# Performance work log

Hardware: AMD Instinct MI355X
Metric: run time of the kernel (lower is better)

The kernel has to match this reference:

```python
import jax, jax.numpy as jnp
import numpy as np

N_NODES = 50000
N_EDGES = 800000
NFEAT = 128
NHID = 128
BN_EPS = 1e-5


def setup_inputs() -> dict:
    key = jax.random.key(0)
    ks = jax.random.split(key, 8)
    x = jax.random.normal(ks[0], (N_NODES, NFEAT), dtype=jnp.float32)
    edge_index = jax.random.randint(ks[1], (2, N_EDGES), 0, N_NODES, dtype=jnp.int64)
    # Linear weights in torch layout [out, in]; scaled like kaiming-ish init.
    W1 = jax.random.normal(ks[2], (NHID, NFEAT), dtype=jnp.float32) / np.sqrt(NFEAT)
    b1 = jax.random.normal(ks[3], (NHID,), dtype=jnp.float32) * 0.01
    gamma = jnp.ones((NHID,), dtype=jnp.float32)
    beta = jnp.zeros((NHID,), dtype=jnp.float32)
    W2 = jax.random.normal(ks[4], (NHID, NHID), dtype=jnp.float32) / np.sqrt(NHID)
    b2 = jax.random.normal(ks[5], (NHID,), dtype=jnp.float32) * 0.01
    return {"x": x, "edge_index": edge_index, "W1": W1, "b1": b1,
            "gamma": gamma, "beta": beta, "W2": W2, "b2": b2}


def reference(x, edge_index, W1, b1, gamma, beta, W2, b2):
    # GINConv, eps = 0: h = (1 + eps) * x + sum_{j in N(i)} x_j
    src, dst = edge_index[0], edge_index[1]
    agg = x + jax.ops.segment_sum(x[src], dst, num_segments=N_NODES)  # [N, nfeat]
    # MLP: Linear -> ReLU -> BatchNorm1d (training stats) -> Linear
    h = jnp.maximum(agg @ W1.T + b1, 0.0)                             # [N, nhid]
    mean = jnp.mean(h, axis=0)
    var = jnp.var(h, axis=0)  # biased variance, as torch BN uses for normalization
    h = (h - mean) * jax.lax.rsqrt(var + BN_EPS) * gamma + beta
    return h @ W2.T + b2
```

## Files before the change

### kernel.cpp

```cpp
#include <hip/hip_runtime.h>

#define N_NODES 50000
#define N_EDGES 800000
#define NF 128
#define BN_EPS 1e-5f
#define G_ROWS 32
#define GBLOCKS ((N_NODES + G_ROWS - 1) / G_ROWS)
#define NB 1568
#define SCAN_BLOCKS ((N_NODES + 255) / 256)
#define AP 136
#define HP 132

typedef __attribute__((ext_vector_type(8))) short short8;
typedef __attribute__((ext_vector_type(4))) float f32x4;

__device__ __forceinline__ unsigned short f2bf(float f) {
    union { float f; unsigned int i; } v; v.f = f;
    unsigned int r = (v.i + 0x7fffu + ((v.i >> 16) & 1u)) >> 16;
    return (unsigned short)r;
}
__device__ __forceinline__ float bf2f(unsigned short u) {
    union { unsigned int i; float f; } v; v.i = ((unsigned int)u) << 16; return v.f;
}

#define SETUP_C (N_NODES * NF / 4)
#define SETUP_P (128 * 128)
#define SETUP_Z N_NODES
#define SETUP_S 256
__global__ void setup_kernel(const float* __restrict__ x, unsigned short* __restrict__ xb,
                             const float* __restrict__ W1, const float* __restrict__ W2,
                             unsigned short* __restrict__ Wb1, unsigned short* __restrict__ Wb2,
                             int* __restrict__ counts, float* __restrict__ stats,
                             int do_convert) {
    int i = blockIdx.x * blockDim.x + threadIdx.x;
    int off = do_convert ? 0 : SETUP_C;
    i += off;
    if (i < SETUP_C) {
        float4 v = ((const float4*)x)[i];
        ushort4 u;
        u.x = f2bf(v.x); u.y = f2bf(v.y); u.z = f2bf(v.z); u.w = f2bf(v.w);
        ((ushort4*)xb)[i] = u;
    } else if (i < SETUP_C + SETUP_P) {
        int j = i - SETUP_C;
        Wb1[j] = f2bf(W1[j]);
        Wb2[j] = f2bf(W2[j]);
    } else if (i < SETUP_C + SETUP_P + SETUP_Z) {
        counts[i - SETUP_C - SETUP_P] = 0;
    } else if (i < SETUP_C + SETUP_P + SETUP_Z + SETUP_S) {
        stats[i - SETUP_C - SETUP_P - SETUP_Z] = 0.0f;
    }
}

__global__ void hist_kernel(const int* __restrict__ ei, int* __restrict__ counts,
                            int* __restrict__ rank) {
    int t = blockIdx.x * blockDim.x + threadIdx.x;
    if (t < N_EDGES) rank[t] = atomicAdd(&counts[ei[N_EDGES + t]], 1);
}

__global__ __launch_bounds__(256) void scan_reduce(const int* __restrict__ counts,
                                                   int* __restrict__ partials) {
    __shared__ int red[256];
    int t = threadIdx.x;
    int i = blockIdx.x * 256 + t;
    red[t] = (i < N_NODES) ? counts[i] : 0;
    __syncthreads();
    for (int off = 128; off > 0; off >>= 1) {
        if (t < off) red[t] += red[t + off];
        __syncthreads();
    }
    if (t == 0) partials[blockIdx.x] = red[0];
}

__global__ __launch_bounds__(256) void scan_partials2(int* __restrict__ partials) {
    __shared__ int s[256];
    int t = threadIdx.x;
    int v = (t < SCAN_BLOCKS) ? partials[t] : 0;
    s[t] = v;
    __syncthreads();
    for (int off = 1; off < 256; off <<= 1) {
        int u = (t >= off) ? s[t - off] : 0;
        __syncthreads();
        s[t] += u;
        __syncthreads();
    }
    if (t < SCAN_BLOCKS) partials[t] = s[t] - v;
}

__global__ __launch_bounds__(256) void scan_apply(const int* __restrict__ counts,
                                                  const int* __restrict__ partials,
                                                  int* __restrict__ rowptr) {
    __shared__ int s[256];
    int t = threadIdx.x;
    int i = blockIdx.x * 256 + t;
    int v = (i < N_NODES) ? counts[i] : 0;
    s[t] = v;
    __syncthreads();
    for (int off = 1; off < 256; off <<= 1) {
        int u = (t >= off) ? s[t - off] : 0;
        __syncthreads();
        s[t] += u;
        __syncthreads();
    }
    int excl = partials[blockIdx.x] + s[t] - v;
    if (i < N_NODES) rowptr[i] = excl;
    if (i == 0) rowptr[N_NODES] = N_EDGES;
}

__global__ void fill_kernel(const int* __restrict__ ei,
                            const int* __restrict__ rowptr,
                            const int* __restrict__ rank,
                            int* __restrict__ ssrc) {
    int t = blockIdx.x * blockDim.x + threadIdx.x;
    if (t < N_EDGES) {
        int dst = ei[N_EDGES + t];
        ssrc[rowptr[dst] + rank[t]] = ei[t];
    }
}

__global__ __launch_bounds__(256) void gather_bf16(const unsigned short* __restrict__ xb,
                                                   const int* __restrict__ rowptr,
                                                   const int* __restrict__ ssrc,
                                                   unsigned short* __restrict__ buf) {
    int node = (blockIdx.x * blockDim.x + threadIdx.x) >> 6;
    int lane = threadIdx.x & 63;
    if (node >= N_NODES) return;
    const unsigned int* x2 = (const unsigned int*)xb;
    unsigned int u = x2[(size_t)node * 64 + lane];
    float ax = bf2f((unsigned short)(u & 0xffffu));
    float ay = bf2f((unsigned short)(u >> 16));
    int beg = rowptr[node], end = rowptr[node + 1];
    int e = beg;
    for (; e + 3 < end; e += 4) {
        int s0 = ssrc[e], s1 = ssrc[e + 1], s2 = ssrc[e + 2], s3 = ssrc[e + 3];
        unsigned int u0 = x2[(size_t)s0 * 64 + lane];
        unsigned int u1 = x2[(size_t)s1 * 64 + lane];
        unsigned int u2 = x2[(size_t)s2 * 64 + lane];
        unsigned int u3 = x2[(size_t)s3 * 64 + lane];
        ax += bf2f((unsigned short)(u0 & 0xffffu)) + bf2f((unsigned short)(u1 & 0xffffu))
            + bf2f((unsigned short)(u2 & 0xffffu)) + bf2f((unsigned short)(u3 & 0xffffu));
        ay += bf2f((unsigned short)(u0 >> 16)) + bf2f((unsigned short)(u1 >> 16))
            + bf2f((unsigned short)(u2 >> 16)) + bf2f((unsigned short)(u3 >> 16));
    }
    for (; e < end; e++) {
        unsigned int u0 = x2[(size_t)ssrc[e] * 64 + lane];
        ax += bf2f((unsigned short)(u0 & 0xffffu));
        ay += bf2f((unsigned short)(u0 >> 16));
    }
    unsigned int packed = ((unsigned int)f2bf(ay) << 16) | (unsigned int)f2bf(ax);
    ((unsigned int*)buf)[(size_t)node * 64 + lane] = packed;
}

__global__ __launch_bounds__(256) void gemm1_bf16(
    unsigned short* __restrict__ buf,
    const unsigned short* __restrict__ Wb,
    const float* __restrict__ b1,
    float* __restrict__ P) {
    __shared__ unsigned short At[G_ROWS][AP];
    __shared__ float Ht[G_ROWS][HP];

    int t = threadIdx.x;
    int base = blockIdx.x * G_ROWS;
    int nrows = N_NODES - base; if (nrows > G_ROWS) nrows = G_ROWS;

    for (int i = t; i < G_ROWS * 16; i += 256) {
        int r = i >> 4, c8 = i & 15;
        uint4 v = make_uint4(0u, 0u, 0u, 0u);
        if (r < nrows) v = ((const uint4*)(buf + (size_t)(base + r) * NF))[c8];
        *((uint4*)&At[r][c8 * 8]) = v;
    }
    __syncthreads();

    int wave = t >> 6, lane = t & 63;
    int m0 = (wave & 1) * 16;
    int n0 = (wave >> 1) * 64;
    int l15 = lane & 15, q = lane >> 4;

    f32x4 acc[4];
#pragma unroll
    for (int i = 0; i < 4; i++) acc[i] = (f32x4){0.f, 0.f, 0.f, 0.f};

#pragma unroll
    for (int kc = 0; kc < 4; kc++) {
        short8 a = *((const short8*)&At[m0 + l15][kc * 32 + q * 8]);
#pragma unroll
        for (int tile = 0; tile < 4; tile++) {
            short8 b = *((const short8*)(Wb + (size_t)(n0 + 16 * tile + l15) * 128 + kc * 32 + q * 8));
            acc[tile] = __builtin_amdgcn_mfma_f32_16x16x32_bf16(a, b, acc[tile], 0, 0, 0);
        }
    }

#pragma unroll
    for (int tile = 0; tile < 4; tile++) {
        int col = n0 + 16 * tile + l15;
        float bias = b1[col];
#pragma unroll
        for (int reg = 0; reg < 4; reg++) {
            int row = q * 4 + reg;
            Ht[m0 + row][col] = fmaxf(acc[tile][reg] + bias, 0.f);
        }
    }
    __syncthreads();

    for (int i = t; i < G_ROWS * 32; i += 256) {
        int r = i >> 5, c4 = i & 31;
        int row = base + r;
        if (row < N_NODES) {
            float4 v = *((const float4*)&Ht[r][c4 * 4]);
            ushort4 u;
            u.x = f2bf(v.x); u.y = f2bf(v.y); u.z = f2bf(v.z); u.w = f2bf(v.w);
            *((ushort4*)(buf + (size_t)row * NF + c4 * 4)) = u;
        }
    }

    {
        int f = t & 127;
        bool issq = (t >= 128);
        float s = 0.f;
        for (int r = 0; r < nrows; r++) {
            float v = Ht[r][f];
            s += issq ? v * v : v;
        }
        P[(size_t)t * NB + blockIdx.x] = s;
    }
}

__global__ __launch_bounds__(256) void bn_reduce(const float* __restrict__ P,
                                                 const float* __restrict__ gamma,
                                                 const float* __restrict__ beta,
                                                 float* __restrict__ ab) {
    __shared__ float s1[256], s2[256];
    int f = blockIdx.x;
    int j = threadIdx.x;
    float a = 0.f, b = 0.f;
    for (int k = j; k < GBLOCKS; k += 256) {
        a += P[(size_t)f * NB + k];
        b += P[(size_t)(128 + f) * NB + k];
    }
    s1[j] = a; s2[j] = b;
    __syncthreads();
    for (int off = 128; off > 0; off >>= 1) {
        if (j < off) { s1[j] += s1[j + off]; s2[j] += s2[j + off]; }
        __syncthreads();
    }
    if (j == 0) {
        float mean = s1[0] * (1.0f / N_NODES);
        float var = s2[0] * (1.0f / N_NODES) - mean * mean;
        float rstd = rsqrtf(var + BN_EPS);
        float aa = gamma[f] * rstd;
        float cc = beta[f] - mean * aa;
        ab[f] = aa;
        ab[128 + f] = cc;
    }
}

__global__ __launch_bounds__(256) void gemm2_bf16(
    const unsigned short* __restrict__ buf,
    const unsigned short* __restrict__ Wb,
    const float* __restrict__ b2,
    const float* __restrict__ ab,
    float* __restrict__ out) {
    __shared__ unsigned short At[G_ROWS][AP];
    __shared__ float Ht[G_ROWS][HP];

    int t = threadIdx.x;
    int base = blockIdx.x * G_ROWS;
    int nrows = N_NODES - base; if (nrows > G_ROWS) nrows = G_ROWS;

    for (int i = t; i < G_ROWS * 32; i += 256) {
        int r = i >> 5, c4 = i & 31;
        ushort4 u = make_ushort4(0, 0, 0, 0);
        if (r < nrows) {
            ushort4 hv = *((const ushort4*)(buf + (size_t)(base + r) * NF + c4 * 4));
            float4 av = ((const float4*)ab)[c4];
            float4 cv = ((const float4*)(ab + 128))[c4];
            u.x = f2bf(bf2f(hv.x) * av.x + cv.x);
            u.y = f2bf(bf2f(hv.y) * av.y + cv.y);
            u.z = f2bf(bf2f(hv.z) * av.z + cv.z);
            u.w = f2bf(bf2f(hv.w) * av.w + cv.w);
        }
        *((ushort4*)&At[r][c4 * 4]) = u;
    }
    __syncthreads();

    int wave = t >> 6, lane = t & 63;
    int m0 = (wave & 1) * 16;
    int n0 = (wave >> 1) * 64;
    int l15 = lane & 15, q = lane >> 4;

    f32x4 acc[4];
#pragma unroll
    for (int i = 0; i < 4; i++) acc[i] = (f32x4){0.f, 0.f, 0.f, 0.f};

#pragma unroll
    for (int kc = 0; kc < 4; kc++) {
        short8 a = *((const short8*)&At[m0 + l15][kc * 32 + q * 8]);
#pragma unroll
        for (int tile = 0; tile < 4; tile++) {
            short8 b = *((const short8*)(Wb + (size_t)(n0 + 16 * tile + l15) * 128 + kc * 32 + q * 8));
            acc[tile] = __builtin_amdgcn_mfma_f32_16x16x32_bf16(a, b, acc[tile], 0, 0, 0);
        }
    }

#pragma unroll
    for (int tile = 0; tile < 4; tile++) {
        int col = n0 + 16 * tile + l15;
        float bias = b2[col];
#pragma unroll
        for (int reg = 0; reg < 4; reg++) {
            int row = q * 4 + reg;
            Ht[m0 + row][col] = acc[tile][reg] + bias;
        }
    }
    __syncthreads();

    for (int i = t; i < G_ROWS * 32; i += 256) {
        int r = i >> 5, c4 = i & 31;
        int row = base + r;
        if (row < N_NODES)
            *((float4*)(out + (size_t)row * NF + c4 * 4)) = *((const float4*)&Ht[r][c4 * 4]);
    }
}

__global__ void finalize_bn(const float* __restrict__ stats,
                            const float* __restrict__ gamma,
                            const float* __restrict__ beta,
                            float* __restrict__ ab) {
    int f = threadIdx.x;
    if (f < 128) {
        float mean = stats[f] * (1.0f / N_NODES);
        float var = stats[128 + f] * (1.0f / N_NODES) - mean * mean;
        float rstd = rsqrtf(var + BN_EPS);
        float a = gamma[f] * rstd;
        float c = beta[f] - mean * a;
        ab[f] = a;
        ab[128 + f] = c;
    }
}

__global__ __launch_bounds__(256) void fused_gather_gemm1_f32(
    const float* __restrict__ xv,
    const int* __restrict__ rowptr,
    const int* __restrict__ ssrc,
    const unsigned short* __restrict__ Wb,
    const float* __restrict__ b1,
    float* __restrict__ hout,
    float* __restrict__ stats) {
    __shared__ unsigned short At[G_ROWS][AP];
    __shared__ float Ht[G_ROWS][HP];

    int t = threadIdx.x;
    int wave = t >> 6, lane = t & 63;
    int base = blockIdx.x * G_ROWS;
    int nrows = N_NODES - base; if (nrows > G_ROWS) nrows = G_ROWS;

    const float2* xf2 = (const float2*)xv;

    for (int nn = 0; nn < 8; nn++) {
        int r = wave * 8 + nn;
        int node = base + r;
        float2 acc = make_float2(0.f, 0.f);
        if (node < N_NODES) {
            acc = xf2[(size_t)node * 64 + lane];
            int beg = rowptr[node], end = rowptr[node + 1];
            for (int e = beg; e < end; e++) {
                float2 v0 = xf2[(size_t)ssrc[e] * 64 + lane];
                acc.x += v0.x;
                acc.y += v0.y;
            }
        }
        unsigned int packed = ((unsigned int)f2bf(acc.y) << 16) | (unsigned int)f2bf(acc.x);
        *((unsigned int*)&At[r][lane * 2]) = packed;
    }
    __syncthreads();

    int m0 = (wave & 1) * 16;
    int n0 = (wave >> 1) * 64;
    int l15 = lane & 15, q = lane >> 4;

    f32x4 acc[4];
#pragma unroll
    for (int i = 0; i < 4; i++) acc[i] = (f32x4){0.f, 0.f, 0.f, 0.f};

#pragma unroll
    for (int kc = 0; kc < 4; kc++) {
        short8 a = *((const short8*)&At[m0 + l15][kc * 32 + q * 8]);
#pragma unroll
        for (int tile = 0; tile < 4; tile++) {
            short8 b = *((const short8*)(Wb + (size_t)(n0 + 16 * tile + l15) * 128 + kc * 32 + q * 8));
            acc[tile] = __builtin_amdgcn_mfma_f32_16x16x32_bf16(a, b, acc[tile], 0, 0, 0);
        }
    }

#pragma unroll
    for (int tile = 0; tile < 4; tile++) {
        int col = n0 + 16 * tile + l15;
        float bias = b1[col];
#pragma unroll
        for (int reg = 0; reg < 4; reg++) {
            int row = q * 4 + reg;
            Ht[m0 + row][col] = fmaxf(acc[tile][reg] + bias, 0.f);
        }
    }
    __syncthreads();

    for (int i = t; i < G_ROWS * 32; i += 256) {
        int r = i >> 5, c4 = i & 31;
        int row = base + r;
        if (row < N_NODES)
            *((float4*)(hout + (size_t)row * NF + c4 * 4)) = *((const float4*)&Ht[r][c4 * 4]);
    }

    if (t < 128) {
        float s = 0.f, sq = 0.f;
        for (int r = 0; r < nrows; r++) {
            float v = Ht[r][t];
            s += v; sq += v * v;
        }
        atomicAdd(&stats[t], s);
        atomicAdd(&stats[128 + t], sq);
    }
}

__global__ __launch_bounds__(256) void gemm2_f32(
    float* __restrict__ h,
    const unsigned short* __restrict__ Wb,
    const float* __restrict__ b2,
    const float* __restrict__ ab) {
    __shared__ unsigned short At[G_ROWS][AP];
    __shared__ float Ht[G_ROWS][HP];

    int t = threadIdx.x;
    int base = blockIdx.x * G_ROWS;
    int nrows = N_NODES - base; if (nrows > G_ROWS) nrows = G_ROWS;

    for (int i = t; i < G_ROWS * 32; i += 256) {
        int r = i >> 5, c4 = i & 31;
        float4 v = make_float4(0.f, 0.f, 0.f, 0.f);
        if (r < nrows) {
            float4 hv = ((const float4*)(h + (size_t)(base + r) * NF))[c4];
            float4 av = ((const float4*)ab)[c4];
            float4 cv = ((const float4*)(ab + 128))[c4];
            v.x = hv.x * av.x + cv.x;
            v.y = hv.y * av.y + cv.y;
            v.z = hv.z * av.z + cv.z;
            v.w = hv.w * av.w + cv.w;
        }
        ushort4 u;
        u.x = f2bf(v.x); u.y = f2bf(v.y); u.z = f2bf(v.z); u.w = f2bf(v.w);
        *((ushort4*)&At[r][c4 * 4]) = u;
    }
    __syncthreads();

    int wave = t >> 6, lane = t & 63;
    int m0 = (wave & 1) * 16;
    int n0 = (wave >> 1) * 64;
    int l15 = lane & 15, q = lane >> 4;

    f32x4 acc[4];
#pragma unroll
    for (int i = 0; i < 4; i++) acc[i] = (f32x4){0.f, 0.f, 0.f, 0.f};

#pragma unroll
    for (int kc = 0; kc < 4; kc++) {
        short8 a = *((const short8*)&At[m0 + l15][kc * 32 + q * 8]);
#pragma unroll
        for (int tile = 0; tile < 4; tile++) {
            short8 b = *((const short8*)(Wb + (size_t)(n0 + 16 * tile + l15) * 128 + kc * 32 + q * 8));
            acc[tile] = __builtin_amdgcn_mfma_f32_16x16x32_bf16(a, b, acc[tile], 0, 0, 0);
        }
    }

#pragma unroll
    for (int tile = 0; tile < 4; tile++) {
        int col = n0 + 16 * tile + l15;
        float bias = b2[col];
#pragma unroll
        for (int reg = 0; reg < 4; reg++) {
            int row = q * 4 + reg;
            Ht[m0 + row][col] = acc[tile][reg] + bias;
        }
    }
    __syncthreads();

    for (int i = t; i < G_ROWS * 32; i += 256) {
        int r = i >> 5, c4 = i & 31;
        int row = base + r;
        if (row < N_NODES)
            *((float4*)(h + (size_t)row * NF + c4 * 4)) = *((const float4*)&Ht[r][c4 * 4]);
    }
}

extern "C" void kernel_launch(void* const* d_in, const int* in_sizes, int n_in,
                              void* d_out, int out_size, void* d_ws, size_t ws_size,
                              hipStream_t stream) {
    const float* x     = (const float*)d_in[0];
    const int*   ei    = (const int*)d_in[1];
    const float* W1    = (const float*)d_in[2];
    const float* b1    = (const float*)d_in[3];
    const float* gamma = (const float*)d_in[4];
    const float* beta  = (const float*)d_in[5];
    const float* W2    = (const float*)d_in[6];
    const float* b2    = (const float*)d_in[7];

    float* out = (float*)d_out;

    float*          stats    = (float*)d_ws;
    float*          ab       = stats + 256;
    float*          P        = ab + 256;
    unsigned short* Wb1      = (unsigned short*)(P + 256 * NB);
    unsigned short* Wb2      = Wb1 + 128 * 128;
    int*            counts   = (int*)(Wb2 + 128 * 128);
    int*            rowptr   = counts + N_NODES;
    int*            partials = rowptr + N_NODES + 1;
    int*            rank     = partials + 256;
    int*            ssrc     = rank + N_EDGES;
    unsigned short* xb       = (unsigned short*)(ssrc + N_EDGES);
    unsigned short* buf      = xb + (size_t)N_NODES * NF;

    size_t need = (size_t)((char*)(buf + (size_t)N_NODES * NF) - (char*)d_ws);
    bool bf16_path = ws_size >= need;

    if (bf16_path) {
        int total = SETUP_C + SETUP_P + SETUP_Z + SETUP_S;
        setup_kernel<<<(total + 255) / 256, 256, 0, stream>>>(
            x, xb, W1, W2, Wb1, Wb2, counts, stats, 1);
    } else {
        int total = SETUP_P + SETUP_Z + SETUP_S;
        setup_kernel<<<(total + 255) / 256, 256, 0, stream>>>(
            x, xb, W1, W2, Wb1, Wb2, counts, stats, 0);
    }
    hist_kernel<<<(N_EDGES + 255) / 256, 256, 0, stream>>>(ei, counts, rank);
    scan_reduce<<<SCAN_BLOCKS, 256, 0, stream>>>(counts, partials);
    scan_partials2<<<1, 256, 0, stream>>>(partials);
    scan_apply<<<SCAN_BLOCKS, 256, 0, stream>>>(counts, partials, rowptr);
    fill_kernel<<<(N_EDGES + 255) / 256, 256, 0, stream>>>(ei, rowptr, rank, ssrc);

    if (bf16_path) {
        gather_bf16<<<(N_NODES * 64) / 256, 256, 0, stream>>>(xb, rowptr, ssrc, buf);
        gemm1_bf16<<<GBLOCKS, 256, 0, stream>>>(buf, Wb1, b1, P);
        bn_reduce<<<128, 256, 0, stream>>>(P, gamma, beta, ab);
        gemm2_bf16<<<GBLOCKS, 256, 0, stream>>>(buf, Wb2, b2, ab, out);
    } else {
        fused_gather_gemm1_f32<<<GBLOCKS, 256, 0, stream>>>(
            x, rowptr, ssrc, Wb1, b1, out, stats);
        finalize_bn<<<1, 128, 0, stream>>>(stats, gamma, beta, ab);
        gemm2_f32<<<GBLOCKS, 256, 0, stream>>>(out, Wb2, b2, ab);
    }
}
```

Baseline: 235.0 us.

## Fuse CSR build into one cooperative kernel and split gather across half-waves

Replaces the six preprocessing launches (bf16 convert, histogram, three-stage scan, fill) with a single cooperative kernel that separates the phases with grid-wide syncs, removing the per-launch gaps. The gather kernel now has each half-wave handle a different neighbor and load 8 bytes per lane, with the two halves combined by a cross-lane shuffle. This aims for more memory parallelism per wave. The cooperative path needs all 1024 blocks resident at once, and its grid syncs add their own cost. It also stops zeroing the stats buffer, which the bf16 path does not appear to use.

New measurement: 755.2 us. 221% more time.

```diff
diff --git a/kernel.cpp b/kernel.cpp
--- a/kernel.cpp
+++ b/kernel.cpp
@@ -1,4 +1,7 @@
 #include <hip/hip_runtime.h>
+#include <hip/hip_cooperative_groups.h>
+
+namespace cg = cooperative_groups;
 
 #define N_NODES 50000
 #define N_EDGES 800000
@@ -10,6 +13,7 @@
 #define SCAN_BLOCKS ((N_NODES + 255) / 256)
 #define AP 136
 #define HP 132
+#define COOP_BLOCKS 1024
 
 typedef __attribute__((ext_vector_type(8))) short short8;
 typedef __attribute__((ext_vector_type(4))) float f32x4;
@@ -22,11 +26,91 @@
 __device__ __forceinline__ float bf2f(unsigned short u) {
     union { unsigned int i; float f; } v; v.i = ((unsigned int)u) << 16; return v.f;
 }
+__device__ __forceinline__ float bflo(unsigned int u) { return bf2f((unsigned short)(u & 0xffffu)); }
+__device__ __forceinline__ float bfhi(unsigned int u) { return bf2f((unsigned short)(u >> 16)); }
 
 #define SETUP_C (N_NODES * NF / 4)
 #define SETUP_P (128 * 128)
-#define SETUP_Z N_NODES
-#define SETUP_S 256
+
+__global__ __launch_bounds__(256) void build_coop(
+    const float* __restrict__ x, unsigned short* __restrict__ xb,
+    const float* __restrict__ W1, const float* __restrict__ W2,
+    unsigned short* __restrict__ Wb1, unsigned short* __restrict__ Wb2,
+    const int* __restrict__ ei, int* __restrict__ counts,
+    int* __restrict__ rank, int* __restrict__ partials,
+    int* __restrict__ rowptr, int* __restrict__ ssrc) {
+    cg::grid_group grid = cg::this_grid();
+    __shared__ int sh[256];
+    int t = threadIdx.x;
+    int gtid = blockIdx.x * 256 + t;
+    int gstride = gridDim.x * 256;
+
+    for (int i = gtid; i < SETUP_C; i += gstride) {
+        float4 v = ((const float4*)x)[i];
+        ushort4 u;
+        u.x = f2bf(v.x); u.y = f2bf(v.y); u.z = f2bf(v.z); u.w = f2bf(v.w);
+        ((ushort4*)xb)[i] = u;
+    }
+    for (int i = gtid; i < SETUP_P; i += gstride) {
+        Wb1[i] = f2bf(W1[i]);
+        Wb2[i] = f2bf(W2[i]);
+    }
+    for (int i = gtid; i < N_NODES; i += gstride) counts[i] = 0;
+    grid.sync();
+
+    for (int e = gtid; e < N_EDGES; e += gstride)
+        rank[e] = atomicAdd(&counts[ei[N_EDGES + e]], 1);
+    grid.sync();
+
+    if (blockIdx.x < SCAN_BLOCKS) {
+        int i = blockIdx.x * 256 + t;
+        sh[t] = (i < N_NODES) ? counts[i] : 0;
+        __syncthreads();
+        for (int off = 128; off > 0; off >>= 1) {
+            if (t < off) sh[t] += sh[t + off];
+            __syncthreads();
+        }
+        if (t == 0) partials[blockIdx.x] = sh[0];
+    }
+    grid.sync();
+
+    if (blockIdx.x == 0) {
+        int v = (t < SCAN_BLOCKS) ? partials[t] : 0;
+        sh[t] = v;
+        __syncthreads();
+        for (int off = 1; off < 256; off <<= 1) {
+            int u = (t >= off) ? sh[t - off] : 0;
+            __syncthreads();
+            sh[t] += u;
+            __syncthreads();
+        }
+        if (t < SCAN_BLOCKS) partials[t] = sh[t] - v;
+    }
+    grid.sync();
+
+    if (blockIdx.x < SCAN_BLOCKS) {
+        int i = blockIdx.x * 256 + t;
+        int v = (i < N_NODES) ? counts[i] : 0;
+        sh[t] = v;
+        __syncthreads();
+        for (int off = 1; off < 256; off <<= 1) {
+            int u = (t >= off) ? sh[t - off] : 0;
+            __syncthreads();
+            sh[t] += u;
+            __syncthreads();
+        }
+        int excl = partials[blockIdx.x] + sh[t] - v;
+        if (i < N_NODES) rowptr[i] = excl;
+        if (i == 0) rowptr[N_NODES] = N_EDGES;
+    }
+    grid.sync();
+
+    for (int e = gtid; e < N_EDGES; e += gstride) {
+        int dst = ei[N_EDGES + e];
+        ssrc[rowptr[dst] + rank[e]] = ei[e];
+    }
+}
+
 __global__ void setup_kernel(const float* __restrict__ x, unsigned short* __restrict__ xb,
                              const float* __restrict__ W1, const float* __restrict__ W2,
                              unsigned short* __restrict__ Wb1, unsigned short* __restrict__ Wb2,
@@ -44,10 +128,10 @@
         int j = i - SETUP_C;
         Wb1[j] = f2bf(W1[j]);
         Wb2[j] = f2bf(W2[j]);
-    } else if (i < SETUP_C + SETUP_P + SETUP_Z) {
+    } else if (i < SETUP_C + SETUP_P + N_NODES) {
         counts[i - SETUP_C - SETUP_P] = 0;
-    } else if (i < SETUP_C + SETUP_P + SETUP_Z + SETUP_S) {
-        stats[i - SETUP_C - SETUP_P - SETUP_Z] = 0.0f;
+    } else if (i < SETUP_C + SETUP_P + N_NODES + 256) {
+        stats[i - SETUP_C - SETUP_P - N_NODES] = 0.0f;
     }
 }
 
@@ -124,30 +208,49 @@
     int node = (blockIdx.x * blockDim.x + threadIdx.x) >> 6;
     int lane = threadIdx.x & 63;
     if (node >= N_NODES) return;
-    const unsigned int* x2 = (const unsigned int*)xb;
-    unsigned int u = x2[(size_t)node * 64 + lane];
-    float ax = bf2f((unsigned short)(u & 0xffffu));
-    float ay = bf2f((unsigned short)(u >> 16));
+    int half = lane >> 5;
+    int fl = lane & 31;
+    const uint2* x4 = (const uint2*)xb;
+
+    float a0 = 0.f, a1 = 0.f, a2 = 0.f, a3 = 0.f;
+    if (half == 0) {
+        uint2 u = x4[(size_t)node * 32 + fl];
+        a0 = bflo(u.x); a1 = bfhi(u.x); a2 = bflo(u.y); a3 = bfhi(u.y);
+    }
     int beg = rowptr[node], end = rowptr[node + 1];
     int e = beg;
     for (; e + 3 < end; e += 4) {
-        int s0 = ssrc[e], s1 = ssrc[e + 1], s2 = ssrc[e + 2], s3 = ssrc[e + 3];
-        unsigned int u0 = x2[(size_t)s0 * 64 + lane];
-        unsigned int u1 = x2[(size_t)s1 * 64 + lane];
-        unsigned int u2 = x2[(size_t)s2 * 64 + lane];
-        unsigned int u3 = x2[(size_t)s3 * 64 + lane];
-        ax += bf2f((unsigned short)(u0 & 0xffffu)) + bf2f((unsigned short)(u1 & 0xffffu))
-            + bf2f((unsigned short)(u2 & 0xffffu)) + bf2f((unsigned short)(u3 & 0xffffu));
-        ay += bf2f((unsigned short)(u0 >> 16)) + bf2f((unsigned short)(u1 >> 16))
-            + bf2f((unsigned short)(u2 >> 16)) + bf2f((unsigned short)(u3 >> 16));
-    }
-    for (; e < end; e++) {
-        unsigned int u0 = x2[(size_t)ssrc[e] * 64 + lane];
-        ax += bf2f((unsigned short)(u0 & 0xffffu));
-        ay += bf2f((unsigned short)(u0 >> 16));
-    }
-    unsigned int packed = ((unsigned int)f2bf(ay) << 16) | (unsigned int)f2bf(ax);
-    ((unsigned int*)buf)[(size_t)node * 64 + lane] = packed;
+        int sA = ssrc[e + half];
+        int sB = ssrc[e + 2 + half];
+        uint2 uA = x4[(size_t)sA * 32 + fl];
+        uint2 uB = x4[(size_t)sB * 32 + fl];
+        a0 += bflo(uA.x) + bflo(uB.x);
+        a1 += bfhi(uA.x) + bfhi(uB.x);
+        a2 += bflo(uA.y) + bflo(uB.y);
+        a3 += bfhi(uA.y) + bfhi(uB.y);
+    }
+    for (; e + 1 < end; e += 2) {
+        int s = ssrc[e + half];
+        uint2 u = x4[(size_t)s * 32 + fl];
+        a0 += bflo(u.x); a1 += bfhi(u.x);
+        a2 += bflo(u.y); a3 += bfhi(u.y);
+    }
+    if (e < end && half == 0) {
+        int s = ssrc[e];
+        uint2 u = x4[(size_t)s * 32 + fl];
+        a0 += bflo(u.x); a1 += bfhi(u.x);
+        a2 += bflo(u.y); a3 += bfhi(u.y);
+    }
+    a0 += __shfl_xor(a0, 32);
+    a1 += __shfl_xor(a1, 32);
+    a2 += __shfl_xor(a2, 32);
+    a3 += __shfl_xor(a3, 32);
+    if (half == 0) {
+        uint2 o;
+        o.x = ((unsigned int)f2bf(a1) << 16) | (unsigned int)f2bf(a0);
+        o.y = ((unsigned int)f2bf(a3) << 16) | (unsigned int)f2bf(a2);
+        ((uint2*)buf)[(size_t)node * 32 + fl] = o;
+    }
 }
 
 __global__ __launch_bounds__(256) void gemm1_bf16(
@@ -520,27 +623,40 @@
     size_t need = (size_t)((char*)(buf + (size_t)N_NODES * NF) - (char*)d_ws);
     bool bf16_path = ws_size >= need;
 
+    int dev = 0, coop_ok = 0;
+    hipGetDevice(&dev);
+    hipDeviceGetAttribute(&coop_ok, hipDeviceAttributeCooperativeLaunch, dev);
+
     if (bf16_path) {
-        int total = SETUP_C + SETUP_P + SETUP_Z + SETUP_S;
-        setup_kernel<<<(total + 255) / 256, 256, 0, stream>>>(
-            x, xb, W1, W2, Wb1, Wb2, counts, stats, 1);
-    } else {
-        int total = SETUP_P + SETUP_Z + SETUP_S;
-        setup_kernel<<<(total + 255) / 256, 256, 0, stream>>>(
-            x, xb, W1, W2, Wb1, Wb2, counts, stats, 0);
-    }
-    hist_kernel<<<(N_EDGES + 255) / 256, 256, 0, stream>>>(ei, counts, rank);
-    scan_reduce<<<SCAN_BLOCKS, 256, 0, stream>>>(counts, partials);
-    scan_partials2<<<1, 256, 0, stream>>>(partials);
-    scan_apply<<<SCAN_BLOCKS, 256, 0, stream>>>(counts, partials, rowptr);
-    fill_kernel<<<(N_EDGES + 255) / 256, 256, 0, stream>>>(ei, rowptr, rank, ssrc);
-
-    if (bf16_path) {
+        if (coop_ok) {
+            void* args[12] = {(void*)&x, (void*)&xb, (void*)&W1, (void*)&W2,
+                              (void*)&Wb1, (void*)&Wb2, (void*)&ei, (void*)&counts,
+                              (void*)&rank, (void*)&partials, (void*)&rowptr, (void*)&ssrc};
+            hipLaunchCooperativeKernel((void*)build_coop, dim3(COOP_BLOCKS), dim3(256),
+                                       args, 0, stream);
+        } else {
+            int total = SETUP_C + SETUP_P + N_NODES + 256;
+            setup_kernel<<<(total + 255) / 256, 256, 0, stream>>>(
+                x, xb, W1, W2, Wb1, Wb2, counts, stats, 1);
+            hist_kernel<<<(N_EDGES + 255) / 256, 256, 0, stream>>>(ei, counts, rank);
+            scan_reduce<<<SCAN_BLOCKS, 256, 0, stream>>>(counts, partials);
+            scan_partials2<<<1, 256, 0, stream>>>(partials);
+            scan_apply<<<SCAN_BLOCKS, 256, 0, stream>>>(counts, partials, rowptr);
+            fill_kernel<<<(N_EDGES + 255) / 256, 256, 0, stream>>>(ei, rowptr, rank, ssrc);
+        }
         gather_bf16<<<(N_NODES * 64) / 256, 256, 0, stream>>>(xb, rowptr, ssrc, buf);
         gemm1_bf16<<<GBLOCKS, 256, 0, stream>>>(buf, Wb1, b1, P);
         bn_reduce<<<128, 256, 0, stream>>>(P, gamma, beta, ab);
         gemm2_bf16<<<GBLOCKS, 256, 0, stream>>>(buf, Wb2, b2, ab, out);
     } else {
+        int total = SETUP_P + N_NODES + 256;
+        setup_kernel<<<(total + 255) / 256, 256, 0, stream>>>(
+            x, xb, W1, W2, Wb1, Wb2, counts, stats, 0);
+        hist_kernel<<<(N_EDGES + 255) / 256, 256, 0, stream>>>(ei, counts, rank);
+        scan_reduce<<<SCAN_BLOCKS, 256, 0, stream>>>(counts, partials);
+        scan_partials2<<<1, 256, 0, stream>>>(partials);
+        scan_apply<<<SCAN_BLOCKS, 256, 0, stream>>>(counts, partials, rowptr);
+        fill_kernel<<<(N_EDGES + 255) / 256, 256, 0, stream>>>(ei, rowptr, rank, ssrc);
         fused_gather_gemm1_f32<<<GBLOCKS, 256, 0, stream>>>(
             x, rowptr, ssrc, Wb1, b1, out, stats);
         finalize_bn<<<1, 128, 0, stream>>>(stats, gamma, beta, ab);
```
